# Optimization experiments

Hardware: AMD Instinct MI355X
Metric: run time of the kernel (lower is better)

The kernel has to match this reference:

```python
import jax, jax.numpy as jnp
import numpy as np

T_STEPS = 4
LAYERS = 10
CYCLE = 10
C = 64
TAU = 1.2
V_TH = 0.5
SG_ALPHA = 4.0  # spikingjelly default surrogate.Sigmoid alpha


@jax.custom_vjp
def heaviside_sg(x):
    return (x >= 0.0).astype(x.dtype)

def _h_fwd(x):
    return heaviside_sg(x), x

def _h_bwd(x, g):
    s = jax.nn.sigmoid(SG_ALPHA * x)
    return (SG_ALPHA * s * (1.0 - s) * g,)

heaviside_sg.defvjp(_h_fwd, _h_bwd)


def lif(x_seq):
    # MultiStepLIFNode: v' = v + (x - (v - v_reset))/tau, hard reset to v_reset=0,
    # detach_reset=True -> spike in reset path is stop-gradient'ed.
    def step(v, x):
        v = v + (x - v) / TAU
        spike = heaviside_sg(v - V_TH)
        v = v * (1.0 - jax.lax.stop_gradient(spike))
        return v, spike
    _, spikes = jax.lax.scan(step, jnp.zeros_like(x_seq[0]), x_seq)
    return spikes


def conv_seq(x, w, b, dilation=1):
    # x: [T,B,Cin,L]; w: [Cout,Cin,K]; 'same' padding for odd K
    T, B, Ci, L = x.shape
    K = w.shape[-1]
    pad = (K - 1) * dilation // 2
    y = jax.lax.conv_general_dilated(
        x.reshape(T * B, Ci, L), w, (1,), [(pad, pad)],
        rhs_dilation=(dilation,), dimension_numbers=('NCH', 'OIH', 'NCH'))
    y = y + b[None, :, None]
    return y.reshape(T, B, -1, L)


def setup_inputs() -> dict:
    key = jax.random.key(0)
    ks = jax.random.split(key, 20)
    B, L = 4, 4096
    s = 0.1
    n = jax.random.normal
    inp = {
        'audio': jax.random.uniform(ks[0], (B, L), dtype=jnp.float32),
        'diffusion_step': jax.random.randint(ks[1], (B,), 0, 50),
        'W_in': n(ks[2], (C, 1, 1), jnp.float32) * s,
        'b_in': n(ks[3], (C,), jnp.float32) * s,
        'demb_w1': n(ks[4], (LAYERS, C, 1), jnp.float32) * s,
        'demb_b1': n(ks[5], (LAYERS, C), jnp.float32) * s,
        'demb_w2': n(ks[6], (LAYERS, C, C), jnp.float32) * s,
        'demb_b2': n(ks[7], (LAYERS, C), jnp.float32) * s,
        'dproj_w': n(ks[8], (LAYERS, C, C), jnp.float32) * s,
        'dproj_b': n(ks[9], (LAYERS, C), jnp.float32) * s,
        'conv_w': n(ks[10], (LAYERS, 2 * C, C, 3), jnp.float32) * 0.05,
        'conv_b': n(ks[11], (LAYERS, 2 * C), jnp.float32) * s,
        'skip_w': n(ks[12], (LAYERS, C, C, 1), jnp.float32) * s,
        'skip_b': n(ks[13], (LAYERS, C), jnp.float32) * s,
        'res_w': n(ks[14], (LAYERS, C, C, 1), jnp.float32) * s,
        'res_b': n(ks[15], (LAYERS, C), jnp.float32) * s,
        'W_out': n(ks[16], (1, C, 1), jnp.float32) * s,
        'b_out': n(ks[17], (1,), jnp.float32) * s,
    }
    return inp


def reference(audio, diffusion_step, W_in, b_in, demb_w1, demb_b1, demb_w2,
              demb_b2, dproj_w, dproj_b, conv_w, conv_b, skip_w, skip_b,
              res_w, res_b, W_out, b_out):
    B, L = audio.shape
    # Poisson encoder: spike = 1[u < x] per timestep (fixed key -> deterministic)
    u = jax.random.uniform(jax.random.key(42), (T_STEPS, B, 1, L), dtype=jnp.float32)
    spike_seq = (u < audio[None, :, None, :]).astype(jnp.float32)

    x = conv_seq(spike_seq, W_in, b_in)          # [T,B,C,L]
    x = lif(x)

    d = diffusion_step.astype(jnp.float32)[:, None]  # [B,1]
    total_skip = jnp.zeros_like(x)
    for i in range(LAYERS):
        dilation = 2 ** (i % CYCLE)
        emb = jax.nn.silu(d @ demb_w1[i].T + demb_b1[i]) @ demb_w2[i].T + demb_b2[i]  # [B,C]
        proj = emb @ dproj_w[i].T + dproj_b[i]                                        # [B,C]
        y = x + proj[None, :, :, None]
        y = conv_seq(y, conv_w[i], conv_b[i], dilation=dilation)  # [T,B,2C,L]
        y = lif(y)
        gate, filt = jnp.split(y, 2, axis=2)
        y = jax.nn.sigmoid(gate) * jnp.tanh(filt)
        total_skip = total_skip + conv_seq(y, skip_w[i], skip_b[i])
        x = x + conv_seq(y, res_w[i], res_b[i])

    total_skip = jax.nn.relu(total_skip)
    out = conv_seq(total_skip, W_out, b_out)  # [T,B,1,L]
    out = lif(out)
    return out.sum(axis=0)  # [B,1,L]
```

## Files before the change

### kernel.cpp

```cpp
#include <hip/hip_runtime.h>

#define LL 4096
#define NB 4
#define NC 64
#define NT 4
#define NLAYERS 10
#define XS 5120
#define XPAD 512

typedef float v2f __attribute__((ext_vector_type(2)));

__device__ __forceinline__ void threefry2x32(unsigned x0, unsigned x1,
                                             unsigned& o0, unsigned& o1) {
  const unsigned ks0 = 0u, ks1 = 42u;
  const unsigned ks2 = 0x1BD11BDAu ^ ks0 ^ ks1;
  const unsigned ks[3] = {ks0, ks1, ks2};
  const unsigned r0[4] = {13u, 15u, 26u, 6u};
  const unsigned r1[4] = {17u, 29u, 16u, 24u};
  x0 += ks0; x1 += ks1;
#pragma unroll
  for (int g = 0; g < 5; ++g) {
    const unsigned* rr = (g & 1) ? r1 : r0;
#pragma unroll
    for (int j = 0; j < 4; ++j) {
      x0 += x1;
      unsigned r = rr[j];
      x1 = (x1 << r) | (x1 >> (32u - r));
      x1 ^= x0;
    }
    x0 += ks[(g + 1) % 3];
    x1 += ks[(g + 2) % 3] + (unsigned)(g + 1);
  }
  o0 = x0; o1 = x1;
}

__device__ __forceinline__ float u01(unsigned bits) {
  return __uint_as_float((bits >> 9) | 0x3f800000u) - 1.0f;
}

__device__ __forceinline__ float lif_step(float& v, float xt) {
  v = v + (xt - v) / 1.2f;
  float s = (v >= 0.5f) ? 1.0f : 0.0f;
  v = v * (1.0f - s);
  return s;
}

__global__ void prep_kernel(const float* __restrict__ skip_w,
                            const float* __restrict__ res_w,
                            const float* __restrict__ conv_w,
                            float* __restrict__ skipT,
                            float* __restrict__ resT,
                            float* __restrict__ wT) {
  int i = blockIdx.x;
  for (int idx = threadIdx.x; idx < 4096; idx += 256) {
    int c = idx >> 6, cp = idx & 63;
    skipT[i * 4096 + cp * 64 + c] = skip_w[i * 4096 + c * 64 + cp];
    resT[i * 4096 + cp * 64 + c] = res_w[i * 4096 + c * 64 + cp];
  }
  for (int idx = threadIdx.x; idx < 16 * 64 * 3 * 8; idx += 256) {
    int col = idx & 7;
    int r = idx >> 3;
    int k = r % 3; r /= 3;
    int ci = r % 64;
    int g = r / 64;
    int co = (col < 4) ? (g * 4 + col) : (64 + g * 4 + (col - 4));
    wT[i * 24576 + idx] = conv_w[(i * 128 + co) * 192 + ci * 3 + k];
  }
}

__global__ void proj_kernel(const int* __restrict__ dstep,
                            const float* __restrict__ w1, const float* __restrict__ b1,
                            const float* __restrict__ w2, const float* __restrict__ b2,
                            const float* __restrict__ pw, const float* __restrict__ pb,
                            float* __restrict__ proj) {
  __shared__ float e1[NB][NC];
  __shared__ float e2[NB][NC];
  int i = blockIdx.x;
  int tid = threadIdx.x;
  int b = tid >> 6, c = tid & 63;
  float d = (float)dstep[b];
  float v = d * w1[i * 64 + c] + b1[i * 64 + c];
  v = v / (1.0f + expf(-v));
  e1[b][c] = v;
  __syncthreads();
  float a = b2[i * 64 + c];
  for (int cp = 0; cp < 64; ++cp) a += e1[b][cp] * w2[(i * 64 + c) * 64 + cp];
  e2[b][c] = a;
  __syncthreads();
  float p = pb[i * 64 + c];
  for (int cp = 0; cp < 64; ++cp) p += e2[b][cp] * pw[(i * 64 + c) * 64 + cp];
  proj[(i * 4 + b) * 64 + c] = p;
}

__global__ void pc_kernel(const float* __restrict__ proj,
                          const float* __restrict__ conv_w,
                          float* __restrict__ pc) {
  __shared__ float pv[64];
  int layer = blockIdx.x, b = blockIdx.y;
  int tid = threadIdx.x;
  if (tid < 64) pv[tid] = proj[(layer * 4 + b) * 64 + tid];
  __syncthreads();
  int co = tid;
  const float* w = conv_w + (layer * 128 + co) * 192;
  float s0 = 0.0f, s1 = 0.0f, s2 = 0.0f;
  for (int ci = 0; ci < 64; ++ci) {
    float p = pv[ci];
    s0 += p * w[ci * 3 + 0];
    s1 += p * w[ci * 3 + 1];
    s2 += p * w[ci * 3 + 2];
  }
  float* o = pc + ((layer * 4 + b) * 128 + co) * 3;
  o[0] = s0; o[1] = s1; o[2] = s2;
}

__global__ void padzero_kernel(float* __restrict__ x) {
  int row = blockIdx.x;
  float* base = x + (size_t)row * XS * 4;
  for (int i = threadIdx.x; i < XPAD; i += 256) {
    *(float4*)&base[i * 4] = float4{0.f, 0.f, 0.f, 0.f};
    *(float4*)&base[(XPAD + LL + i) * 4] = float4{0.f, 0.f, 0.f, 0.f};
  }
}

__global__ void encode_lif_kernel(const float* __restrict__ audio,
                                  const float* __restrict__ W_in,
                                  const float* __restrict__ b_in,
                                  float* __restrict__ x) {
  int tid = threadIdx.x;
  int lq = tid & 63, grp = tid >> 6;
  int l = blockIdx.x * 64 + lq;
  int b = blockIdx.y;
  float a = audio[b * LL + l];
  unsigned p0 = (unsigned)(b * LL + l);
  unsigned p1 = 16384u + p0;
  unsigned o00, o01, o10, o11;
  threefry2x32(p0, p0 + 32768u, o00, o01);
  threefry2x32(p1, p1 + 32768u, o10, o11);
  float sp[4];
  sp[0] = (u01(o00) < a) ? 1.0f : 0.0f;
  sp[1] = (u01(o10) < a) ? 1.0f : 0.0f;
  sp[2] = (u01(o01) < a) ? 1.0f : 0.0f;
  sp[3] = (u01(o11) < a) ? 1.0f : 0.0f;
  for (int j = 0; j < 16; ++j) {
    int c = grp * 16 + j;
    float w = W_in[c], bb = b_in[c];
    float v = 0.0f;
    float4 o;
    float* op = (float*)&o;
#pragma unroll
    for (int t = 0; t < 4; ++t) op[t] = lif_step(v, w * sp[t] + bb);
    *(float4*)&x[(size_t)((b * 64 + c) * XS + XPAD + l) * 4] = o;
  }
}

template <int DIL>
__global__ __launch_bounds__(256) void layer_conv_kernel(
    const float* __restrict__ x, const float* __restrict__ wT,
    const float* __restrict__ conv_b, const float* __restrict__ pc,
    float* __restrict__ y, int layer) {
  __shared__ float w_lds[192 * 8];
  int tid = threadIdx.x;
  int g = blockIdx.y;
  int b = blockIdx.z;
  int l = blockIdx.x * 256 + tid;
  const float* wbase = wT + (size_t)(layer * 16 + g) * 1536;

  for (int idx = tid; idx < 1536; idx += 256) w_lds[idx] = wbase[idx];
  __syncthreads();

  const float* px = x + (size_t)(b * 64 * XS + XPAD + l) * 4;

  v2f ag[8], af[8];
#pragma unroll
  for (int q = 0; q < 8; ++q) {
    ag[q] = (v2f)(0.0f);
    af[q] = (v2f)(0.0f);
  }

  float4 xa[3], xb[3];
  auto loadx = [&](float4* dst) {
    dst[0] = *(const float4*)(px - (size_t)DIL * 4);
    dst[1] = *(const float4*)px;
    dst[2] = *(const float4*)(px + (size_t)DIL * 4);
    px += (size_t)XS * 4;
  };
  auto compute = [&](int ci, const float4* xv) {
#pragma unroll
    for (int k = 0; k < 3; ++k) {
      const v2f* wp = (const v2f*)&w_lds[(ci * 3 + k) * 8];
      v2f g0 = wp[0], g1 = wp[1];
      v2f f0 = wp[2], f1 = wp[3];
      const float* xk = (const float*)&xv[k];
#pragma unroll
      for (int t = 0; t < 4; ++t) {
        float xq = xk[t];
        v2f x2;
        x2.x = xq; x2.y = xq;
        ag[t * 2 + 0] += g0 * x2;
        ag[t * 2 + 1] += g1 * x2;
        af[t * 2 + 0] += f0 * x2;
        af[t * 2 + 1] += f1 * x2;
      }
    }
  };

  loadx(xa);
  for (int ci = 0; ci < 64; ci += 2) {
    loadx(xb);
    compute(ci, xa);
    if (ci + 2 < 64) loadx(xa);
    compute(ci + 1, xb);
  }

  const float SIG1 = 0.73105857863000489f;
  const float TANH1 = 0.76159415595576486f;
  bool lb = (l < DIL), rb = (l >= LL - DIL);
#pragma unroll
  for (int j = 0; j < 4; ++j) {
    int cog = g * 4 + j;
    int cof = 64 + g * 4 + j;
    const float* pg = pc + ((layer * 4 + b) * 128 + cog) * 3;
    const float* pf = pc + ((layer * 4 + b) * 128 + cof) * 3;
    float S0g = pg[0], S1g = pg[1], S2g = pg[2];
    float S0f = pf[0], S1f = pf[1], S2f = pf[2];
    float bg = conv_b[layer * 128 + cog] + S0g + S1g + S2g;
    float bf = conv_b[layer * 128 + cof] + S0f + S1f + S2f;
    bg -= (lb ? S0g : 0.0f) + (rb ? S2g : 0.0f);
    bf -= (lb ? S0f : 0.0f) + (rb ? S2f : 0.0f);
    float vg = 0.0f, vf = 0.0f;
    float4 o;
    float* op = (float*)&o;
#pragma unroll
    for (int t = 0; t < 4; ++t) {
      float av = ag[t * 2 + (j >> 1)][j & 1];
      float fv = af[t * 2 + (j >> 1)][j & 1];
      float sg = lif_step(vg, av + bg);
      float sf = lif_step(vf, fv + bf);
      float gv = (sg != 0.0f) ? SIG1 : 0.5f;
      float tv = (sf != 0.0f) ? TANH1 : 0.0f;
      op[t] = gv * tv;
    }
    *(float4*)&y[(size_t)((b * 64 + cog) * LL + l) * 4] = o;
  }
}

__global__ __launch_bounds__(256) void skip_res_kernel(
    const float* __restrict__ y, const float* __restrict__ skipT,
    const float* __restrict__ resT, const float* __restrict__ skip_b,
    const float* __restrict__ res_b, float* __restrict__ tskip,
    float* __restrict__ x, int layer) {
  int tid = threadIdx.x;
  int lg = tid & 31;
  int cg = tid >> 5;
  int cv = blockIdx.y;
  int b = blockIdx.z;
  int l0 = blockIdx.x * 32 + lg;
  int c0 = cg * 8;

  const float* wsrc = (cv ? resT : skipT) + layer * 4096 + c0;
  const float* yb = y + (size_t)(b * 64 * LL + l0) * 4;

  v2f acc[16];
#pragma unroll
  for (int q = 0; q < 16; ++q) acc[q] = (v2f)(0.0f);

  float4 w0a = *(const float4*)&wsrc[0];
  float4 w1a = *(const float4*)&wsrc[4];
  float4 y0a = *(const float4*)yb;

  for (int cp = 0; cp < 64; ++cp) {
    int cpn = (cp < 63) ? cp + 1 : 63;
    float4 w0b = *(const float4*)&wsrc[cpn * 64];
    float4 w1b = *(const float4*)&wsrc[cpn * 64 + 4];
    float4 y0b = *(const float4*)(yb + (size_t)cpn * LL * 4);

    float wv[8] = {w0a.x, w0a.y, w0a.z, w0a.w, w1a.x, w1a.y, w1a.z, w1a.w};
    const v2f* yp0 = (const v2f*)&y0a;
#pragma unroll
    for (int i = 0; i < 8; ++i) {
      v2f w2;
      w2.x = wv[i]; w2.y = wv[i];
      acc[i * 2 + 0] += w2 * yp0[0];
      acc[i * 2 + 1] += w2 * yp0[1];
    }
    w0a = w0b; w1a = w1b; y0a = y0b;
  }

  const float* bsrc = (cv ? res_b : skip_b) + layer * 64 + c0;
#pragma unroll
  for (int i = 0; i < 8; ++i) {
    float bb = bsrc[i];
    float r[4];
    r[0] = acc[i * 2 + 0][0] + bb;
    r[1] = acc[i * 2 + 0][1] + bb;
    r[2] = acc[i * 2 + 1][0] + bb;
    r[3] = acc[i * 2 + 1][1] + bb;
    if (cv == 0) {
      size_t idx = (size_t)((b * 64 + c0 + i) * LL + l0) * 4;
      float4 o0;
      if (layer == 0) {
        o0 = float4{0.f, 0.f, 0.f, 0.f};
      } else {
        o0 = *(const float4*)&tskip[idx];
      }
      o0.x += r[0]; o0.y += r[1]; o0.z += r[2]; o0.w += r[3];
      *(float4*)&tskip[idx] = o0;
    } else {
      size_t idx = (size_t)((b * 64 + c0 + i) * XS + XPAD + l0) * 4;
      float4 o0 = *(const float4*)&x[idx];
      o0.x += r[0]; o0.y += r[1]; o0.z += r[2]; o0.w += r[3];
      *(float4*)&x[idx] = o0;
    }
  }
}

__global__ void out_kernel(const float* __restrict__ tskip,
                           const float* __restrict__ W_out,
                           const float* __restrict__ b_out,
                           float* __restrict__ out) {
  __shared__ float red[4][4][64];
  int tid = threadIdx.x;
  int lq = tid & 63, grp = tid >> 6;
  int l = blockIdx.x * 64 + lq;
  int b = blockIdx.y;
  float acc[4] = {0.0f, 0.0f, 0.0f, 0.0f};
  for (int j = 0; j < 16; ++j) {
    int c = grp * 16 + j;
    float w = W_out[c];
    float4 sv = *(const float4*)&tskip[(size_t)((b * 64 + c) * LL + l) * 4];
    acc[0] += fmaxf(sv.x, 0.0f) * w;
    acc[1] += fmaxf(sv.y, 0.0f) * w;
    acc[2] += fmaxf(sv.z, 0.0f) * w;
    acc[3] += fmaxf(sv.w, 0.0f) * w;
  }
#pragma unroll
  for (int t = 0; t < 4; ++t) red[grp][t][lq] = acc[t];
  __syncthreads();
  if (grp == 0) {
    float bo = b_out[0];
    float v = 0.0f, s = 0.0f;
#pragma unroll
    for (int t = 0; t < 4; ++t) {
      float a = red[0][t][lq] + red[1][t][lq] + red[2][t][lq] + red[3][t][lq] + bo;
      s += lif_step(v, a);
    }
    out[b * LL + l] = s;
  }
}

extern "C" void kernel_launch(void* const* d_in, const int* in_sizes, int n_in,
                              void* d_out, int out_size, void* d_ws, size_t ws_size,
                              hipStream_t stream) {
  const float* audio   = (const float*)d_in[0];
  const int*   dstep   = (const int*)d_in[1];
  const float* W_in    = (const float*)d_in[2];
  const float* b_in    = (const float*)d_in[3];
  const float* demb_w1 = (const float*)d_in[4];
  const float* demb_b1 = (const float*)d_in[5];
  const float* demb_w2 = (const float*)d_in[6];
  const float* demb_b2 = (const float*)d_in[7];
  const float* dproj_w = (const float*)d_in[8];
  const float* dproj_b = (const float*)d_in[9];
  const float* conv_w  = (const float*)d_in[10];
  const float* conv_b  = (const float*)d_in[11];
  const float* skip_w  = (const float*)d_in[12];
  const float* skip_b  = (const float*)d_in[13];
  const float* res_w   = (const float*)d_in[14];
  const float* res_b   = (const float*)d_in[15];
  const float* W_out   = (const float*)d_in[16];
  const float* b_out   = (const float*)d_in[17];
  float* out = (float*)d_out;
  float* ws = (float*)d_ws;

  float* proj  = ws;
  float* skipT = proj + 2560;
  float* resT  = skipT + 40960;
  float* pc    = resT + 40960;
  float* wT    = pc + 15360;
  float* x     = wT + 245760;
  float* y     = x + 5242880;
  float* tskip = y + 4194304;

  prep_kernel<<<10, 256, 0, stream>>>(skip_w, res_w, conv_w, skipT, resT, wT);
  proj_kernel<<<10, 256, 0, stream>>>(dstep, demb_w1, demb_b1, demb_w2, demb_b2,
                                      dproj_w, dproj_b, proj);
  pc_kernel<<<dim3(10, 4), 128, 0, stream>>>(proj, conv_w, pc);
  padzero_kernel<<<256, 256, 0, stream>>>(x);
  encode_lif_kernel<<<dim3(64, 4), 256, 0, stream>>>(audio, W_in, b_in, x);

  for (int i = 0; i < NLAYERS; ++i) {
    dim3 gc(16, 16, 4);
    switch (i) {
      case 0: layer_conv_kernel<1><<<gc, 256, 0, stream>>>(x, wT, conv_b, pc, y, i); break;
      case 1: layer_conv_kernel<2><<<gc, 256, 0, stream>>>(x, wT, conv_b, pc, y, i); break;
      case 2: layer_conv_kernel<4><<<gc, 256, 0, stream>>>(x, wT, conv_b, pc, y, i); break;
      case 3: layer_conv_kernel<8><<<gc, 256, 0, stream>>>(x, wT, conv_b, pc, y, i); break;
      case 4: layer_conv_kernel<16><<<gc, 256, 0, stream>>>(x, wT, conv_b, pc, y, i); break;
      case 5: layer_conv_kernel<32><<<gc, 256, 0, stream>>>(x, wT, conv_b, pc, y, i); break;
      case 6: layer_conv_kernel<64><<<gc, 256, 0, stream>>>(x, wT, conv_b, pc, y, i); break;
      case 7: layer_conv_kernel<128><<<gc, 256, 0, stream>>>(x, wT, conv_b, pc, y, i); break;
      case 8: layer_conv_kernel<256><<<gc, 256, 0, stream>>>(x, wT, conv_b, pc, y, i); break;
      case 9: layer_conv_kernel<512><<<gc, 256, 0, stream>>>(x, wT, conv_b, pc, y, i); break;
    }
    skip_res_kernel<<<dim3(128, 2, 4), 256, 0, stream>>>(y, skipT, resT, skip_b,
                                                         res_b, tskip, x, i);
  }
  out_kernel<<<dim3(64, 4), 256, 0, stream>>>(tskip, W_out, b_out, out);
}
```

Baseline: 893.1 us.

## Fuse dilated conv+LIF with skip/residual 1x1 convs per layer via LDS

```diff
diff --git a/kernel.cpp b/kernel.cpp
--- a/kernel.cpp
+++ b/kernel.cpp
@@ -113,9 +113,9 @@
   o[0] = s0; o[1] = s1; o[2] = s2;
 }
 
-__global__ void padzero_kernel(float* __restrict__ x) {
+__global__ void padzero_kernel(float* __restrict__ x0, float* __restrict__ x1) {
   int row = blockIdx.x;
-  float* base = x + (size_t)row * XS * 4;
+  float* base = (row < 256 ? x0 : x1) + (size_t)(row & 255) * XS * 4;
   for (int i = threadIdx.x; i < XPAD; i += 256) {
     *(float4*)&base[i * 4] = float4{0.f, 0.f, 0.f, 0.f};
     *(float4*)&base[(XPAD + LL + i) * 4] = float4{0.f, 0.f, 0.f, 0.f};
@@ -154,162 +154,166 @@
 }
 
 template <int DIL>
-__global__ __launch_bounds__(256) void layer_conv_kernel(
-    const float* __restrict__ x, const float* __restrict__ wT,
-    const float* __restrict__ conv_b, const float* __restrict__ pc,
-    float* __restrict__ y, int layer) {
-  __shared__ float w_lds[192 * 8];
+__global__ __launch_bounds__(256, 4) void fused_layer_kernel(
+    const float* __restrict__ xin, float* __restrict__ xout,
+    const float* __restrict__ wT, const float* __restrict__ conv_b,
+    const float* __restrict__ pc, const float* __restrict__ skipT,
+    const float* __restrict__ resT, const float* __restrict__ skip_b,
+    const float* __restrict__ res_b, float* __restrict__ tskip, int layer) {
+  __shared__ float y_lds[64][17][4];
   int tid = threadIdx.x;
-  int g = blockIdx.y;
-  int b = blockIdx.z;
-  int l = blockIdx.x * 256 + tid;
-  const float* wbase = wT + (size_t)(layer * 16 + g) * 1536;
-
-  for (int idx = tid; idx < 1536; idx += 256) w_lds[idx] = wbase[idx];
+  int lq = tid & 15;
+  int grp = tid >> 4;
+  int b = blockIdx.y;
+  int l = blockIdx.x * 16 + lq;
+
+  {
+    const float* wbase = wT + (size_t)(layer * 16 + grp) * 1536;
+    const float* px = xin + (size_t)((b * 64) * XS + XPAD + l) * 4;
+
+    v2f ag[8], af[8];
+#pragma unroll
+    for (int qq = 0; qq < 8; ++qq) {
+      ag[qq] = (v2f)(0.0f);
+      af[qq] = (v2f)(0.0f);
+    }
+
+    float4 xa[3], xb[3];
+    auto loadx = [&](float4* dst) {
+      dst[0] = *(const float4*)(px - (size_t)DIL * 4);
+      dst[1] = *(const float4*)px;
+      dst[2] = *(const float4*)(px + (size_t)DIL * 4);
+      px += (size_t)XS * 4;
+    };
+    auto compute = [&](int ci, const float4* xv) {
+#pragma unroll
+      for (int k = 0; k < 3; ++k) {
+        float4 gq = *(const float4*)&wbase[(ci * 3 + k) * 8];
+        float4 fq = *(const float4*)&wbase[(ci * 3 + k) * 8 + 4];
+        v2f g0, g1, f0, f1;
+        g0.x = gq.x; g0.y = gq.y; g1.x = gq.z; g1.y = gq.w;
+        f0.x = fq.x; f0.y = fq.y; f1.x = fq.z; f1.y = fq.w;
+        const float* xk = (const float*)&xv[k];
+#pragma unroll
+        for (int t = 0; t < 4; ++t) {
+          float xq = xk[t];
+          v2f x2;
+          x2.x = xq; x2.y = xq;
+          ag[t * 2 + 0] += g0 * x2;
+          ag[t * 2 + 1] += g1 * x2;
+          af[t * 2 + 0] += f0 * x2;
+          af[t * 2 + 1] += f1 * x2;
+        }
+      }
+    };
+
+    loadx(xa);
+    for (int ci = 0; ci < 64; ci += 2) {
+      loadx(xb);
+      compute(ci, xa);
+      if (ci + 2 < 64) loadx(xa);
+      compute(ci + 1, xb);
+    }
+
+    const float SIG1 = 0.73105857863000489f;
+    const float TANH1 = 0.76159415595576486f;
+    bool lb = (l < DIL), rb = (l >= LL - DIL);
+#pragma unroll
+    for (int j = 0; j < 4; ++j) {
+      int cog = grp * 4 + j;
+      int cof = 64 + grp * 4 + j;
+      const float* pg = pc + ((layer * 4 + b) * 128 + cog) * 3;
+      const float* pf = pc + ((layer * 4 + b) * 128 + cof) * 3;
+      float S0g = pg[0], S1g = pg[1], S2g = pg[2];
+      float S0f = pf[0], S1f = pf[1], S2f = pf[2];
+      float bg = conv_b[layer * 128 + cog] + S0g + S1g + S2g;
+      float bf = conv_b[layer * 128 + cof] + S0f + S1f + S2f;
+      bg -= (lb ? S0g : 0.0f) + (rb ? S2g : 0.0f);
+      bf -= (lb ? S0f : 0.0f) + (rb ? S2f : 0.0f);
+      float vg = 0.0f, vf = 0.0f;
+      float4 o;
+      float* op = (float*)&o;
+#pragma unroll
+      for (int t = 0; t < 4; ++t) {
+        float av = ag[t * 2 + (j >> 1)][j & 1];
+        float fv = af[t * 2 + (j >> 1)][j & 1];
+        float sg = lif_step(vg, av + bg);
+        float sf = lif_step(vf, fv + bf);
+        float gv = (sg != 0.0f) ? SIG1 : 0.5f;
+        float tv = (sf != 0.0f) ? TANH1 : 0.0f;
+        op[t] = gv * tv;
+      }
+      *(float4*)&y_lds[cog][lq][0] = o;
+    }
+  }
+
   __syncthreads();
 
-  const float* px = x + (size_t)(b * 64 * XS + XPAD + l) * 4;
-
-  v2f ag[8], af[8];
-#pragma unroll
-  for (int q = 0; q < 8; ++q) {
-    ag[q] = (v2f)(0.0f);
-    af[q] = (v2f)(0.0f);
-  }
-
-  float4 xa[3], xb[3];
-  auto loadx = [&](float4* dst) {
-    dst[0] = *(const float4*)(px - (size_t)DIL * 4);
-    dst[1] = *(const float4*)px;
-    dst[2] = *(const float4*)(px + (size_t)DIL * 4);
-    px += (size_t)XS * 4;
-  };
-  auto compute = [&](int ci, const float4* xv) {
-#pragma unroll
-    for (int k = 0; k < 3; ++k) {
-      const v2f* wp = (const v2f*)&w_lds[(ci * 3 + k) * 8];
-      v2f g0 = wp[0], g1 = wp[1];
-      v2f f0 = wp[2], f1 = wp[3];
-      const float* xk = (const float*)&xv[k];
-#pragma unroll
-      for (int t = 0; t < 4; ++t) {
-        float xq = xk[t];
-        v2f x2;
-        x2.x = xq; x2.y = xq;
-        ag[t * 2 + 0] += g0 * x2;
-        ag[t * 2 + 1] += g1 * x2;
-        af[t * 2 + 0] += f0 * x2;
-        af[t * 2 + 1] += f1 * x2;
+  {
+    int c0 = grp * 4;
+    const float* sw = skipT + layer * 4096 + c0;
+    const float* rw = resT + layer * 4096 + c0;
+
+    v2f as[8], ar[8];
+#pragma unroll
+    for (int qq = 0; qq < 8; ++qq) {
+      as[qq] = (v2f)(0.0f);
+      ar[qq] = (v2f)(0.0f);
+    }
+
+    float4 wsa = *(const float4*)&sw[0];
+    float4 wra = *(const float4*)&rw[0];
+    for (int cp = 0; cp < 64; ++cp) {
+      int cpn = (cp < 63) ? cp + 1 : 63;
+      float4 wsb = *(const float4*)&sw[cpn * 64];
+      float4 wrb = *(const float4*)&rw[cpn * 64];
+      float4 yv = *(const float4*)&y_lds[cp][lq][0];
+      v2f yp0, yp1;
+      yp0.x = yv.x; yp0.y = yv.y;
+      yp1.x = yv.z; yp1.y = yv.w;
+      float wsv[4] = {wsa.x, wsa.y, wsa.z, wsa.w};
+      float wrv[4] = {wra.x, wra.y, wra.z, wra.w};
+#pragma unroll
+      for (int i = 0; i < 4; ++i) {
+        v2f w2s, w2r;
+        w2s.x = wsv[i]; w2s.y = wsv[i];
+        w2r.x = wrv[i]; w2r.y = wrv[i];
+        as[i * 2 + 0] += w2s * yp0;
+        as[i * 2 + 1] += w2s * yp1;
+        ar[i * 2 + 0] += w2r * yp0;
+        ar[i * 2 + 1] += w2r * yp1;
       }
-    }
-  };
-
-  loadx(xa);
-  for (int ci = 0; ci < 64; ci += 2) {
-    loadx(xb);
-    compute(ci, xa);
-    if (ci + 2 < 64) loadx(xa);
-    compute(ci + 1, xb);
-  }
-
-  const float SIG1 = 0.73105857863000489f;
-  const float TANH1 = 0.76159415595576486f;
-  bool lb = (l < DIL), rb = (l >= LL - DIL);
-#pragma unroll
-  for (int j = 0; j < 4; ++j) {
-    int cog = g * 4 + j;
-    int cof = 64 + g * 4 + j;
-    const float* pg = pc + ((layer * 4 + b) * 128 + cog) * 3;
-    const float* pf = pc + ((layer * 4 + b) * 128 + cof) * 3;
-    float S0g = pg[0], S1g = pg[1], S2g = pg[2];
-    float S0f = pf[0], S1f = pf[1], S2f = pf[2];
-    float bg = conv_b[layer * 128 + cog] + S0g + S1g + S2g;
-    float bf = conv_b[layer * 128 + cof] + S0f + S1f + S2f;
-    bg -= (lb ? S0g : 0.0f) + (rb ? S2g : 0.0f);
-    bf -= (lb ? S0f : 0.0f) + (rb ? S2f : 0.0f);
-    float vg = 0.0f, vf = 0.0f;
-    float4 o;
-    float* op = (float*)&o;
-#pragma unroll
-    for (int t = 0; t < 4; ++t) {
-      float av = ag[t * 2 + (j >> 1)][j & 1];
-      float fv = af[t * 2 + (j >> 1)][j & 1];
-      float sg = lif_step(vg, av + bg);
-      float sf = lif_step(vf, fv + bf);
-      float gv = (sg != 0.0f) ? SIG1 : 0.5f;
-      float tv = (sf != 0.0f) ? TANH1 : 0.0f;
-      op[t] = gv * tv;
-    }
-    *(float4*)&y[(size_t)((b * 64 + cog) * LL + l) * 4] = o;
-  }
-}
-
-__global__ __launch_bounds__(256) void skip_res_kernel(
-    const float* __restrict__ y, const float* __restrict__ skipT,
-    const float* __restrict__ resT, const float* __restrict__ skip_b,
-    const float* __restrict__ res_b, float* __restrict__ tskip,
-    float* __restrict__ x, int layer) {
-  int tid = threadIdx.x;
-  int lg = tid & 31;
-  int cg = tid >> 5;
-  int cv = blockIdx.y;
-  int b = blockIdx.z;
-  int l0 = blockIdx.x * 32 + lg;
-  int c0 = cg * 8;
-
-  const float* wsrc = (cv ? resT : skipT) + layer * 4096 + c0;
-  const float* yb = y + (size_t)(b * 64 * LL + l0) * 4;
-
-  v2f acc[16];
-#pragma unroll
-  for (int q = 0; q < 16; ++q) acc[q] = (v2f)(0.0f);
-
-  float4 w0a = *(const float4*)&wsrc[0];
-  float4 w1a = *(const float4*)&wsrc[4];
-  float4 y0a = *(const float4*)yb;
-
-  for (int cp = 0; cp < 64; ++cp) {
-    int cpn = (cp < 63) ? cp + 1 : 63;
-    float4 w0b = *(const float4*)&wsrc[cpn * 64];
-    float4 w1b = *(const float4*)&wsrc[cpn * 64 + 4];
-    float4 y0b = *(const float4*)(yb + (size_t)cpn * LL * 4);
-
-    float wv[8] = {w0a.x, w0a.y, w0a.z, w0a.w, w1a.x, w1a.y, w1a.z, w1a.w};
-    const v2f* yp0 = (const v2f*)&y0a;
-#pragma unroll
-    for (int i = 0; i < 8; ++i) {
-      v2f w2;
-      w2.x = wv[i]; w2.y = wv[i];
-      acc[i * 2 + 0] += w2 * yp0[0];
-      acc[i * 2 + 1] += w2 * yp0[1];
-    }
-    w0a = w0b; w1a = w1b; y0a = y0b;
-  }
-
-  const float* bsrc = (cv ? res_b : skip_b) + layer * 64 + c0;
-#pragma unroll
-  for (int i = 0; i < 8; ++i) {
-    float bb = bsrc[i];
-    float r[4];
-    r[0] = acc[i * 2 + 0][0] + bb;
-    r[1] = acc[i * 2 + 0][1] + bb;
-    r[2] = acc[i * 2 + 1][0] + bb;
-    r[3] = acc[i * 2 + 1][1] + bb;
-    if (cv == 0) {
-      size_t idx = (size_t)((b * 64 + c0 + i) * LL + l0) * 4;
-      float4 o0;
-      if (layer == 0) {
-        o0 = float4{0.f, 0.f, 0.f, 0.f};
-      } else {
-        o0 = *(const float4*)&tskip[idx];
+      wsa = wsb; wra = wrb;
+    }
+
+#pragma unroll
+    for (int i = 0; i < 4; ++i) {
+      int c = c0 + i;
+      float sb = skip_b[layer * 64 + c];
+      float rbv = res_b[layer * 64 + c];
+      {
+        size_t idx = (size_t)((b * 64 + c) * LL + l) * 4;
+        float4 o0;
+        if (layer == 0) {
+          o0 = float4{0.f, 0.f, 0.f, 0.f};
+        } else {
+          o0 = *(const float4*)&tskip[idx];
+        }
+        o0.x += as[i * 2 + 0][0] + sb;
+        o0.y += as[i * 2 + 0][1] + sb;
+        o0.z += as[i * 2 + 1][0] + sb;
+        o0.w += as[i * 2 + 1][1] + sb;
+        *(float4*)&tskip[idx] = o0;
       }
-      o0.x += r[0]; o0.y += r[1]; o0.z += r[2]; o0.w += r[3];
-      *(float4*)&tskip[idx] = o0;
-    } else {
-      size_t idx = (size_t)((b * 64 + c0 + i) * XS + XPAD + l0) * 4;
-      float4 o0 = *(const float4*)&x[idx];
-      o0.x += r[0]; o0.y += r[1]; o0.z += r[2]; o0.w += r[3];
-      *(float4*)&x[idx] = o0;
+      {
+        size_t idx = (size_t)((b * 64 + c) * XS + XPAD + l) * 4;
+        float4 o0 = *(const float4*)&xin[idx];
+        o0.x += ar[i * 2 + 0][0] + rbv;
+        o0.y += ar[i * 2 + 0][1] + rbv;
+        o0.z += ar[i * 2 + 1][0] + rbv;
+        o0.w += ar[i * 2 + 1][1] + rbv;
+        *(float4*)&xout[idx] = o0;
+      }
     }
   }
 }
@@ -377,33 +381,34 @@
   float* resT  = skipT + 40960;
   float* pc    = resT + 40960;
   float* wT    = pc + 15360;
-  float* x     = wT + 245760;
-  float* y     = x + 5242880;
-  float* tskip = y + 4194304;
+  float* x0    = wT + 245760;
+  float* x1    = x0 + 5242880;
+  float* tskip = x1 + 5242880;
 
   prep_kernel<<<10, 256, 0, stream>>>(skip_w, res_w, conv_w, skipT, resT, wT);
   proj_kernel<<<10, 256, 0, stream>>>(dstep, demb_w1, demb_b1, demb_w2, demb_b2,
                                       dproj_w, dproj_b, proj);
   pc_kernel<<<dim3(10, 4), 128, 0, stream>>>(proj, conv_w, pc);
-  padzero_kernel<<<256, 256, 0, stream>>>(x);
-  encode_lif_kernel<<<dim3(64, 4), 256, 0, stream>>>(audio, W_in, b_in, x);
-
+  padzero_kernel<<<512, 256, 0, stream>>>(x0, x1);
+  encode_lif_kernel<<<dim3(64, 4), 256, 0, stream>>>(audio, W_in, b_in, x0);
+
+  float* xcur = x0;
+  float* xnxt = x1;
   for (int i = 0; i < NLAYERS; ++i) {
-    dim3 gc(16, 16, 4);
+    dim3 gc(256, 4);
     switch (i) {
-      case 0: layer_conv_kernel<1><<<gc, 256, 0, stream>>>(x, wT, conv_b, pc, y, i); break;
-      case 1: layer_conv_kernel<2><<<gc, 256, 0, stream>>>(x, wT, conv_b, pc, y, i); break;
-      case 2: layer_conv_kernel<4><<<gc, 256, 0, stream>>>(x, wT, conv_b, pc, y, i); break;
-      case 3: layer_conv_kernel<8><<<gc, 256, 0, stream>>>(x, wT, conv_b, pc, y, i); break;
-      case 4: layer_conv_kernel<16><<<gc, 256, 0, stream>>>(x, wT, conv_b, pc, y, i); break;
-      case 5: layer_conv_kernel<32><<<gc, 256, 0, stream>>>(x, wT, conv_b, pc, y, i); break;
-      case 6: layer_conv_kernel<64><<<gc, 256, 0, stream>>>(x, wT, conv_b, pc, y, i); break;
-      case 7: layer_conv_kernel<128><<<gc, 256, 0, stream>>>(x, wT, conv_b, pc, y, i); break;
-      case 8: layer_conv_kernel<256><<<gc, 256, 0, stream>>>(x, wT, conv_b, pc, y, i); break;
-      case 9: layer_conv_kernel<512><<<gc, 256, 0, stream>>>(x, wT, conv_b, pc, y, i); break;
-    }
-    skip_res_kernel<<<dim3(128, 2, 4), 256, 0, stream>>>(y, skipT, resT, skip_b,
-                                                         res_b, tskip, x, i);
+      case 0: fused_layer_kernel<1><<<gc, 256, 0, stream>>>(xcur, xnxt, wT, conv_b, pc, skipT, resT, skip_b, res_b, tskip, i); break;
+      case 1: fused_layer_kernel<2><<<gc, 256, 0, stream>>>(xcur, xnxt, wT, conv_b, pc, skipT, resT, skip_b, res_b, tskip, i); break;
+      case 2: fused_layer_kernel<4><<<gc, 256, 0, stream>>>(xcur, xnxt, wT, conv_b, pc, skipT, resT, skip_b, res_b, tskip, i); break;
+      case 3: fused_layer_kernel<8><<<gc, 256, 0, stream>>>(xcur, xnxt, wT, conv_b, pc, skipT, resT, skip_b, res_b, tskip, i); break;
+      case 4: fused_layer_kernel<16><<<gc, 256, 0, stream>>>(xcur, xnxt, wT, conv_b, pc, skipT, resT, skip_b, res_b, tskip, i); break;
+      case 5: fused_layer_kernel<32><<<gc, 256, 0, stream>>>(xcur, xnxt, wT, conv_b, pc, skipT, resT, skip_b, res_b, tskip, i); break;
+      case 6: fused_layer_kernel<64><<<gc, 256, 0, stream>>>(xcur, xnxt, wT, conv_b, pc, skipT, resT, skip_b, res_b, tskip, i); break;
+      case 7: fused_layer_kernel<128><<<gc, 256, 0, stream>>>(xcur, xnxt, wT, conv_b, pc, skipT, resT, skip_b, res_b, tskip, i); break;
+      case 8: fused_layer_kernel<256><<<gc, 256, 0, stream>>>(xcur, xnxt, wT, conv_b, pc, skipT, resT, skip_b, res_b, tskip, i); break;
+      case 9: fused_layer_kernel<512><<<gc, 256, 0, stream>>>(xcur, xnxt, wT, conv_b, pc, skipT, resT, skip_b, res_b, tskip, i); break;
+    }
+    float* tmp = xcur; xcur = xnxt; xnxt = tmp;
   }
   out_kernel<<<dim3(64, 4), 256, 0, stream>>>(tskip, W_out, b_out, out);
 }
```

Result: slower. 1.049 ms (+17.5%).
